# Optimization experiments

Measured on AMD Instinct MI355X. Metric: run time of the kernel, lower is better.

## Reference

```python
import jax, jax.numpy as jnp
import numpy as np


def setup_inputs() -> dict:
    key = jax.random.key(0)
    k1, k2, k3 = jax.random.split(key, 3)
    # N, C, H, W per input_specs
    x = jax.random.normal(k1, (16, 8, 1024, 1024), dtype=jnp.float32)
    # weight: (out_channels, in_channels, kH, kW)
    weight = jax.random.normal(k2, (8, 8, 3, 3), dtype=jnp.float32) * 0.1
    bias = jax.random.normal(k3, (8,), dtype=jnp.float32) * 0.1
    return {"x": x, "weight": weight, "bias": bias}


def reference(x, weight, bias):
    # DietConv2dV2's tiled per-kernel-column matmul loop is mathematically a
    # standard direct conv2d (stride=1, padding=1) followed by a bias add.
    out = jax.lax.conv_general_dilated(
        x, weight,
        window_strides=(1, 1),
        padding=((1, 1), (1, 1)),
        dimension_numbers=("NCHW", "OIHW", "NCHW"),
    )
    return out + bias[None, :, None, None]
```

## Files before the change

### kernel.cpp

```cpp
#include <hip/hip_runtime.h>
#include <hip/hip_bf16.h>


typedef __attribute__((ext_vector_type(8))) short short8;
typedef __attribute__((ext_vector_type(4))) float f32x4;

#define HH 1024
#define WW 1024
#define HWsz (1024*1024)
#define WB 64
#define HB 8
#define SROWS 10
#define UROW 72
#define NIT 16
#define NSITES (SROWS*UROW)

__device__ __forceinline__ int pk2(float a, float b) {
    __hip_bfloat162 h = __float22bfloat162_rn(make_float2(a, b));
    return *reinterpret_cast<int*>(&h);
}
__device__ __forceinline__ unsigned short f2bf(float f) {
    unsigned u = __float_as_uint(f);
    return (unsigned short)((u + 0x7FFFu + ((u >> 16) & 1u)) >> 16);
}

__global__ __launch_bounds__(256) void conv3x3_pack2(
    const float* __restrict__ x,
    const float* __restrict__ wgt,
    const float* __restrict__ bias,
    float* __restrict__ out)
{
    __shared__ int4 bfA[NSITES];
    __shared__ int4 bfB[NSITES];

    const int tid  = threadIdx.x;
    const int lane = tid & 63;
    const int wv   = tid >> 6;
    const int l15  = lane & 15;
    const int ch   = lane >> 4;

    const int wx    = blockIdx.x;
    const int strip = blockIdx.y;
    const int n     = blockIdx.z;
    const int w0    = wx * WB;
    const int htbase = strip * (NIT * HB);

    const float* xn = x + (size_t)n * 8 * HWsz;
    const float* base0 = xn + 0 * (size_t)HWsz;
    const float* base1 = xn + 1 * (size_t)HWsz;
    const float* base2 = xn + 2 * (size_t)HWsz;
    const float* base3 = xn + 3 * (size_t)HWsz;
    const float* base4 = xn + 4 * (size_t)HWsz;
    const float* base5 = xn + 5 * (size_t)HWsz;
    const float* base6 = xn + 6 * (size_t)HWsz;
    const float* base7 = xn + 7 * (size_t)HWsz;

    const int s0 = 8 * ch,      kh0 = s0 / 24, kw0 = (s0 % 24) / 8;
    const int s1 = 32 + 8 * ch, kh1 = s1 / 24, kw1 = (s1 % 24) / 8;
    const int s2 = 64 + 8 * ch, kh2 = s2 / 24, kw2 = (s2 % 24) / 8;
    const int off0 = kh0 * UROW + kw0 + 3;
    const int off1 = kh1 * UROW + kw1 + 3;
    const int off2 = kh2 * UROW + kw2 + 3;

    const int hi  = l15 >> 3;
    const int co8 = l15 & 7;
    short8 b0, b1, b2;
    {
        const int ke0 = kh0 - hi, ke1 = kh1 - hi, ke2 = kh2 - hi;
        const bool v0 = (ke0 >= 0) && (ke0 <= 2);
        const bool v1 = (ke1 >= 0) && (ke1 <= 2);
        const bool v2 = (ke2 >= 0) && (ke2 <= 2);
#pragma unroll
        for (int j = 0; j < 8; ++j) {
            b0[j] = (short)(v0 ? f2bf(wgt[co8 * 72 + j * 9 + ke0 * 3 + kw0]) : 0);
            b1[j] = (short)(v1 ? f2bf(wgt[co8 * 72 + j * 9 + ke1 * 3 + kw1]) : 0);
            b2[j] = (short)(v2 ? f2bf(wgt[co8 * 72 + j * 9 + ke2 * 3 + kw2]) : 0);
        }
    }
    const float bv = bias[co8];

    int srow[3], gwc[3];
    bool wok[3], sv[3];
#pragma unroll
    for (int j = 0; j < 3; ++j) {
        const int s = tid + j * 256;
        sv[j]   = (s < NSITES);
        const int r = s / UROW;
        const int u = s - r * UROW;
        srow[j] = r;
        const int gwr = w0 - 4 + u;
        wok[j]  = ((unsigned)gwr < (unsigned)WW);
        gwc[j]  = (gwr < 0) ? 0 : ((gwr > WW - 1) ? WW - 1 : gwr);
    }

    float bkA[3][8], bkB[3][8];

#define LOADS(htile, bk)                                                     \
    {                                                                        \
        _Pragma("unroll")                                                    \
        for (int j = 0; j < 3; ++j) {                                        \
            const int gr  = (htile) - 1 + srow[j];                           \
            const int ghc = (gr < 0) ? 0 : ((gr > HH - 1) ? HH - 1 : gr);    \
            const unsigned voff = ((unsigned)(ghc * WW + gwc[j])) * 4u;      \
            asm volatile("global_load_dword %0, %8, %9\n\t"                  \
                         "global_load_dword %1, %8, %10\n\t"                 \
                         "global_load_dword %2, %8, %11\n\t"                 \
                         "global_load_dword %3, %8, %12\n\t"                 \
                         "global_load_dword %4, %8, %13\n\t"                 \
                         "global_load_dword %5, %8, %14\n\t"                 \
                         "global_load_dword %6, %8, %15\n\t"                 \
                         "global_load_dword %7, %8, %16"                     \
                         : "=v"(bk[j][0]), "=v"(bk[j][1]), "=v"(bk[j][2]),   \
                           "=v"(bk[j][3]), "=v"(bk[j][4]), "=v"(bk[j][5]),   \
                           "=v"(bk[j][6]), "=v"(bk[j][7])                    \
                         : "v"(voff), "s"(base0), "s"(base1), "s"(base2),    \
                           "s"(base3), "s"(base4), "s"(base5), "s"(base6),   \
                           "s"(base7)                                        \
                         : "memory");                                        \
        }                                                                    \
    }

#define CONV(htile, bk, bfb)                                                 \
    {                                                                        \
        _Pragma("unroll")                                                    \
        for (int j = 0; j < 3; ++j) {                                        \
            if (sv[j]) {                                                     \
                const int gr = (htile) - 1 + srow[j];                        \
                const bool ok = ((unsigned)gr < (unsigned)HH) && wok[j];     \
                const float v0 = ok ? bk[j][0] : 0.0f;                       \
                const float v1 = ok ? bk[j][1] : 0.0f;                       \
                const float v2 = ok ? bk[j][2] : 0.0f;                       \
                const float v3 = ok ? bk[j][3] : 0.0f;                       \
                const float v4 = ok ? bk[j][4] : 0.0f;                       \
                const float v5 = ok ? bk[j][5] : 0.0f;                       \
                const float v6 = ok ? bk[j][6] : 0.0f;                       \
                const float v7 = ok ? bk[j][7] : 0.0f;                       \
                int4 pk;                                                     \
                pk.x = pk2(v0, v1);                                          \
                pk.y = pk2(v2, v3);                                          \
                pk.z = pk2(v4, v5);                                          \
                pk.w = pk2(v6, v7);                                          \
                (bfb)[tid + j * 256] = pk;                                   \
            }                                                                \
        }                                                                    \
    }

#define BODY(htile, bsrc)                                                    \
    {                                                                        \
        f32x4 acc[4];                                                        \
        _Pragma("unroll")                                                    \
        for (int wt = 0; wt < 4; ++wt) {                                     \
            acc[wt].x = bv; acc[wt].y = bv; acc[wt].z = bv; acc[wt].w = bv;  \
        }                                                                    \
        const int ub = (2 * wv) * UROW + l15;                                \
        _Pragma("unroll")                                                    \
        for (int wt = 0; wt < 4; ++wt) {                                     \
            const int u = ub + wt * 16;                                      \
            short8 a0 = *reinterpret_cast<const short8*>(&(bsrc)[u + off0]); \
            short8 a1 = *reinterpret_cast<const short8*>(&(bsrc)[u + off1]); \
            short8 a2 = *reinterpret_cast<const short8*>(&(bsrc)[u + off2]); \
            f32x4 c = acc[wt];                                               \
            c = __builtin_amdgcn_mfma_f32_16x16x32_bf16(a0, b0, c, 0, 0, 0); \
            c = __builtin_amdgcn_mfma_f32_16x16x32_bf16(a1, b1, c, 0, 0, 0); \
            c = __builtin_amdgcn_mfma_f32_16x16x32_bf16(a2, b2, c, 0, 0, 0); \
            acc[wt] = c;                                                     \
        }                                                                    \
        float* op = out + ((size_t)n * 8 + co8) * HWsz                       \
                        + (size_t)((htile) + 2 * wv + hi) * WW + w0 + ch * 4;\
        _Pragma("unroll")                                                    \
        for (int wt = 0; wt < 4; ++wt)                                       \
            *reinterpret_cast<float4*>(op + wt * 16) =                       \
                *reinterpret_cast<const float4*>(&acc[wt]);                  \
    }

    LOADS(htbase, bkA);

    for (int k = 0; k < NIT; k += 2) {
        {
            const int ht = htbase + k * HB;
            LOADS(ht + HB, bkB);
            if (k == 0) {
                asm volatile("s_waitcnt vmcnt(24)" ::: "memory");
            } else {
                asm volatile("s_waitcnt vmcnt(28)" ::: "memory");
            }
            __builtin_amdgcn_sched_barrier(0);
            CONV(ht, bkA, bfA);
            asm volatile("s_waitcnt lgkmcnt(0)" ::: "memory");
            __builtin_amdgcn_sched_barrier(0);
            __builtin_amdgcn_s_barrier();
            BODY(ht, bfA);
        }
        {
            const int ht = htbase + (k + 1) * HB;
            int t2 = k + 2; if (t2 > NIT - 1) t2 = NIT - 1;
            LOADS(htbase + t2 * HB, bkA);
            asm volatile("s_waitcnt vmcnt(28)" ::: "memory");
            __builtin_amdgcn_sched_barrier(0);
            CONV(ht, bkB, bfB);
            asm volatile("s_waitcnt lgkmcnt(0)" ::: "memory");
            __builtin_amdgcn_sched_barrier(0);
            __builtin_amdgcn_s_barrier();
            BODY(ht, bfB);
        }
    }
#undef LOADS
#undef CONV
#undef BODY
}

extern "C" void kernel_launch(void* const* d_in, const int* in_sizes, int n_in,
                              void* d_out, int out_size, void* d_ws, size_t ws_size,
                              hipStream_t stream) {
    const float* x    = (const float*)d_in[0];
    const float* wgt  = (const float*)d_in[1];
    const float* bias = (const float*)d_in[2];
    float* out = (float*)d_out;

    dim3 grid(16, 8, 16);
    dim3 block(256, 1, 1);
    conv3x3_pack2<<<grid, block, 0, stream>>>(x, wgt, bias, out);
}
```

Before: 275.3 us.

## Make each wavefront stage its own private LDS halo tile, removing block barriers

Each of the four wavefronts now loads and packs its own 4-row by 56-column bf16 halo region into a private LDS slice. Because no wavefront reads another's data, the per-tile s_barrier is dropped. The width per block shrinks from 64 to 48 columns over a 22-block grid, with the last block shifted to overlap the right edge. In exchange, every wavefront re-reads the rows its neighbours also need and loads more redundant halo columns, so global traffic per output goes up. The waitcnt thresholds are retuned for the extra loads.

New measurement: 373.2 us. 35.6% more time.

```diff
diff --git a/kernel.cpp b/kernel.cpp
--- a/kernel.cpp
+++ b/kernel.cpp
@@ -8,12 +8,13 @@
 #define HH 1024
 #define WW 1024
 #define HWsz (1024*1024)
-#define WB 64
+#define WVW 48
 #define HB 8
-#define SROWS 10
-#define UROW 72
+#define URL 56
+#define RPW 4
+#define SPW (RPW*URL)
 #define NIT 16
-#define NSITES (SROWS*UROW)
+#define GX 22
 
 __device__ __forceinline__ int pk2(float a, float b) {
     __hip_bfloat162 h = __float22bfloat162_rn(make_float2(a, b));
@@ -24,14 +25,13 @@
     return (unsigned short)((u + 0x7FFFu + ((u >> 16) & 1u)) >> 16);
 }
 
-__global__ __launch_bounds__(256) void conv3x3_pack2(
+__global__ __launch_bounds__(256) void conv3x3_wp2(
     const float* __restrict__ x,
     const float* __restrict__ wgt,
     const float* __restrict__ bias,
     float* __restrict__ out)
 {
-    __shared__ int4 bfA[NSITES];
-    __shared__ int4 bfB[NSITES];
+    __shared__ int4 lds[4 * SPW];
 
     const int tid  = threadIdx.x;
     const int lane = tid & 63;
@@ -42,8 +42,9 @@
     const int wx    = blockIdx.x;
     const int strip = blockIdx.y;
     const int n     = blockIdx.z;
-    const int w0    = wx * WB;
+    const int w0    = (wx == GX - 1) ? (WW - WVW) : wx * WVW;
     const int htbase = strip * (NIT * HB);
+    const int rowg0  = 2 * wv - 1;
 
     const float* xn = x + (size_t)n * 8 * HWsz;
     const float* base0 = xn + 0 * (size_t)HWsz;
@@ -58,9 +59,9 @@
     const int s0 = 8 * ch,      kh0 = s0 / 24, kw0 = (s0 % 24) / 8;
     const int s1 = 32 + 8 * ch, kh1 = s1 / 24, kw1 = (s1 % 24) / 8;
     const int s2 = 64 + 8 * ch, kh2 = s2 / 24, kw2 = (s2 % 24) / 8;
-    const int off0 = kh0 * UROW + kw0 + 3;
-    const int off1 = kh1 * UROW + kw1 + 3;
-    const int off2 = kh2 * UROW + kw2 + 3;
+    const int off0 = kh0 * URL + kw0 + 3;
+    const int off1 = kh1 * URL + kw1 + 3;
+    const int off2 = kh2 * URL + kw2 + 3;
 
     const int hi  = l15 >> 3;
     const int co8 = l15 & 7;
@@ -79,27 +80,28 @@
     }
     const float bv = bias[co8];
 
-    int srow[3], gwc[3];
-    bool wok[3], sv[3];
+    int srow[4], gwc[4], lidx[4];
+    bool wok[4];
 #pragma unroll
-    for (int j = 0; j < 3; ++j) {
-        const int s = tid + j * 256;
-        sv[j]   = (s < NSITES);
-        const int r = s / UROW;
-        const int u = s - r * UROW;
+    for (int j = 0; j < 4; ++j) {
+        int s = j * 64 + lane;
+        if (s > SPW - 1) s = SPW - 1;
+        const int r  = s / URL;
+        const int u  = s - r * URL;
         srow[j] = r;
+        lidx[j] = wv * SPW + s;
         const int gwr = w0 - 4 + u;
         wok[j]  = ((unsigned)gwr < (unsigned)WW);
         gwc[j]  = (gwr < 0) ? 0 : ((gwr > WW - 1) ? WW - 1 : gwr);
     }
 
-    float bkA[3][8], bkB[3][8];
-
-#define LOADS(htile, bk)                                                     \
+    float bkA[4][8], bkB[4][8];
+
+#define LOADS(ht, bk)                                                        \
     {                                                                        \
         _Pragma("unroll")                                                    \
-        for (int j = 0; j < 3; ++j) {                                        \
-            const int gr  = (htile) - 1 + srow[j];                           \
+        for (int j = 0; j < 4; ++j) {                                        \
+            const int gr  = (ht) + rowg0 + srow[j];                          \
             const int ghc = (gr < 0) ? 0 : ((gr > HH - 1) ? HH - 1 : gr);    \
             const unsigned voff = ((unsigned)(ghc * WW + gwc[j])) * 4u;      \
             asm volatile("global_load_dword %0, %8, %9\n\t"                  \
@@ -110,9 +112,9 @@
                          "global_load_dword %5, %8, %14\n\t"                 \
                          "global_load_dword %6, %8, %15\n\t"                 \
                          "global_load_dword %7, %8, %16"                     \
-                         : "=v"(bk[j][0]), "=v"(bk[j][1]), "=v"(bk[j][2]),   \
-                           "=v"(bk[j][3]), "=v"(bk[j][4]), "=v"(bk[j][5]),   \
-                           "=v"(bk[j][6]), "=v"(bk[j][7])                    \
+                         : "=&v"(bk[j][0]), "=&v"(bk[j][1]), "=&v"(bk[j][2]),\
+                           "=&v"(bk[j][3]), "=&v"(bk[j][4]), "=&v"(bk[j][5]),\
+                           "=&v"(bk[j][6]), "=&v"(bk[j][7])                  \
                          : "v"(voff), "s"(base0), "s"(base1), "s"(base2),    \
                            "s"(base3), "s"(base4), "s"(base5), "s"(base6),   \
                            "s"(base7)                                        \
@@ -120,45 +122,43 @@
         }                                                                    \
     }
 
-#define CONV(htile, bk, bfb)                                                 \
+#define CONV(ht, bk)                                                         \
     {                                                                        \
         _Pragma("unroll")                                                    \
-        for (int j = 0; j < 3; ++j) {                                        \
-            if (sv[j]) {                                                     \
-                const int gr = (htile) - 1 + srow[j];                        \
-                const bool ok = ((unsigned)gr < (unsigned)HH) && wok[j];     \
-                const float v0 = ok ? bk[j][0] : 0.0f;                       \
-                const float v1 = ok ? bk[j][1] : 0.0f;                       \
-                const float v2 = ok ? bk[j][2] : 0.0f;                       \
-                const float v3 = ok ? bk[j][3] : 0.0f;                       \
-                const float v4 = ok ? bk[j][4] : 0.0f;                       \
-                const float v5 = ok ? bk[j][5] : 0.0f;                       \
-                const float v6 = ok ? bk[j][6] : 0.0f;                       \
-                const float v7 = ok ? bk[j][7] : 0.0f;                       \
-                int4 pk;                                                     \
-                pk.x = pk2(v0, v1);                                          \
-                pk.y = pk2(v2, v3);                                          \
-                pk.z = pk2(v4, v5);                                          \
-                pk.w = pk2(v6, v7);                                          \
-                (bfb)[tid + j * 256] = pk;                                   \
-            }                                                                \
-        }                                                                    \
-    }
-
-#define BODY(htile, bsrc)                                                    \
+        for (int j = 0; j < 4; ++j) {                                        \
+            const int gr = (ht) + rowg0 + srow[j];                           \
+            const bool ok = ((unsigned)gr < (unsigned)HH) && wok[j];         \
+            const float v0 = ok ? bk[j][0] : 0.0f;                           \
+            const float v1 = ok ? bk[j][1] : 0.0f;                           \
+            const float v2 = ok ? bk[j][2] : 0.0f;                           \
+            const float v3 = ok ? bk[j][3] : 0.0f;                           \
+            const float v4 = ok ? bk[j][4] : 0.0f;                           \
+            const float v5 = ok ? bk[j][5] : 0.0f;                           \
+            const float v6 = ok ? bk[j][6] : 0.0f;                           \
+            const float v7 = ok ? bk[j][7] : 0.0f;                           \
+            int4 pk;                                                         \
+            pk.x = pk2(v0, v1);                                              \
+            pk.y = pk2(v2, v3);                                              \
+            pk.z = pk2(v4, v5);                                              \
+            pk.w = pk2(v6, v7);                                              \
+            lds[lidx[j]] = pk;                                               \
+        }                                                                    \
+    }
+
+#define BODY(ht)                                                             \
     {                                                                        \
-        f32x4 acc[4];                                                        \
-        _Pragma("unroll")                                                    \
-        for (int wt = 0; wt < 4; ++wt) {                                     \
+        f32x4 acc[3];                                                        \
+        _Pragma("unroll")                                                    \
+        for (int wt = 0; wt < 3; ++wt) {                                     \
             acc[wt].x = bv; acc[wt].y = bv; acc[wt].z = bv; acc[wt].w = bv;  \
         }                                                                    \
-        const int ub = (2 * wv) * UROW + l15;                                \
-        _Pragma("unroll")                                                    \
-        for (int wt = 0; wt < 4; ++wt) {                                     \
+        const int ub = wv * SPW + l15;                                       \
+        _Pragma("unroll")                                                    \
+        for (int wt = 0; wt < 3; ++wt) {                                     \
             const int u = ub + wt * 16;                                      \
-            short8 a0 = *reinterpret_cast<const short8*>(&(bsrc)[u + off0]); \
-            short8 a1 = *reinterpret_cast<const short8*>(&(bsrc)[u + off1]); \
-            short8 a2 = *reinterpret_cast<const short8*>(&(bsrc)[u + off2]); \
+            short8 a0 = *reinterpret_cast<const short8*>(&lds[u + off0]);    \
+            short8 a1 = *reinterpret_cast<const short8*>(&lds[u + off1]);    \
+            short8 a2 = *reinterpret_cast<const short8*>(&lds[u + off2]);    \
             f32x4 c = acc[wt];                                               \
             c = __builtin_amdgcn_mfma_f32_16x16x32_bf16(a0, b0, c, 0, 0, 0); \
             c = __builtin_amdgcn_mfma_f32_16x16x32_bf16(a1, b1, c, 0, 0, 0); \
@@ -166,9 +166,9 @@
             acc[wt] = c;                                                     \
         }                                                                    \
         float* op = out + ((size_t)n * 8 + co8) * HWsz                       \
-                        + (size_t)((htile) + 2 * wv + hi) * WW + w0 + ch * 4;\
-        _Pragma("unroll")                                                    \
-        for (int wt = 0; wt < 4; ++wt)                                       \
+                        + (size_t)((ht) + 2 * wv + hi) * WW + w0 + ch * 4;   \
+        _Pragma("unroll")                                                    \
+        for (int wt = 0; wt < 3; ++wt)                                       \
             *reinterpret_cast<float4*>(op + wt * 16) =                       \
                 *reinterpret_cast<const float4*>(&acc[wt]);                  \
     }
@@ -180,28 +180,26 @@
             const int ht = htbase + k * HB;
             LOADS(ht + HB, bkB);
             if (k == 0) {
-                asm volatile("s_waitcnt vmcnt(24)" ::: "memory");
+                asm volatile("s_waitcnt vmcnt(32)" ::: "memory");
             } else {
-                asm volatile("s_waitcnt vmcnt(28)" ::: "memory");
+                asm volatile("s_waitcnt vmcnt(35)" ::: "memory");
             }
             __builtin_amdgcn_sched_barrier(0);
-            CONV(ht, bkA, bfA);
+            CONV(ht, bkA);
             asm volatile("s_waitcnt lgkmcnt(0)" ::: "memory");
             __builtin_amdgcn_sched_barrier(0);
-            __builtin_amdgcn_s_barrier();
-            BODY(ht, bfA);
+            BODY(ht);
         }
         {
             const int ht = htbase + (k + 1) * HB;
             int t2 = k + 2; if (t2 > NIT - 1) t2 = NIT - 1;
             LOADS(htbase + t2 * HB, bkA);
-            asm volatile("s_waitcnt vmcnt(28)" ::: "memory");
-            __builtin_amdgcn_sched_barrier(0);
-            CONV(ht, bkB, bfB);
+            asm volatile("s_waitcnt vmcnt(35)" ::: "memory");
+            __builtin_amdgcn_sched_barrier(0);
+            CONV(ht, bkB);
             asm volatile("s_waitcnt lgkmcnt(0)" ::: "memory");
             __builtin_amdgcn_sched_barrier(0);
-            __builtin_amdgcn_s_barrier();
-            BODY(ht, bfB);
+            BODY(ht);
         }
     }
 #undef LOADS
@@ -217,7 +215,7 @@
     const float* bias = (const float*)d_in[2];
     float* out = (float*)d_out;
 
-    dim3 grid(16, 8, 16);
+    dim3 grid(GX, 8, 16);
     dim3 block(256, 1, 1);
-    conv3x3_pack2<<<grid, block, 0, stream>>>(x, wgt, bias, out);
-}
+    conv3x3_wp2<<<grid, block, 0, stream>>>(x, wgt, bias, out);
+}
```
